# Optimization experiments

Hardware: AMD Instinct MI355X
Metric: run time of the kernel (lower is better)

Reference implementation:

```python
import jax, jax.numpy as jnp
import numpy as np

EMBED_DIM = 1024
HEAD_SIZE = 64
B, T = 4, 4096


def setup_inputs() -> dict:
    key = jax.random.key(0)
    kx, kq, kk, kv = jax.random.split(key, 4)
    x = jax.random.normal(kx, (B, T, EMBED_DIM), dtype=jnp.float32)
    sw = 1.0 / np.sqrt(EMBED_DIM)  # kaiming-ish init scale for linear weights
    Wq = jax.random.normal(kq, (EMBED_DIM, HEAD_SIZE), dtype=jnp.float32) * sw
    Wk = jax.random.normal(kk, (EMBED_DIM, HEAD_SIZE), dtype=jnp.float32) * sw
    Wv = jax.random.normal(kv, (EMBED_DIM, HEAD_SIZE), dtype=jnp.float32) * sw
    return {"x": x, "Wq": Wq, "Wk": Wk, "Wv": Wv}


def reference(x, Wq, Wk, Wv):
    Bn, Tn, C = x.shape
    q = jnp.einsum('btc,ch->bth', x, Wq)
    k = jnp.einsum('btc,ch->bth', x, Wk)
    v = jnp.einsum('btc,ch->bth', x, Wv)
    # NOTE: original scales by sqrt(C) = sqrt(embed_dim), not sqrt(head_size)
    scale = 1.0 / jnp.sqrt(jnp.asarray(C, dtype=x.dtype))
    wei = jnp.einsum('bth,bsh->bts', q, k) * scale  # [B, T, T]
    causal = jnp.tril(jnp.ones((Tn, Tn), dtype=bool))
    wei = jnp.where(causal, wei, -jnp.inf)
    wei = jax.nn.softmax(wei, axis=-1)
    # dropout p=0.0 (eval mode): identity
    return jnp.einsum('bts,bsh->bth', wei, v)
```

## Files before the change

kernel.cpp:

```cpp
#include <hip/hip_runtime.h>
#include <cstdint>


typedef __bf16 bf16;
typedef __bf16 bf16x4 __attribute__((ext_vector_type(4)));
typedef __bf16 bf16x8 __attribute__((ext_vector_type(8)));
typedef float  f32x4  __attribute__((ext_vector_type(4)));

#define MFMA16(a, b, c) __builtin_amdgcn_mfma_f32_16x16x32_bf16((a), (b), (c), 0, 0, 0)

#if __has_builtin(__builtin_amdgcn_exp2f)
#define EXP2(x) __builtin_amdgcn_exp2f(x)
#else
#define EXP2(x) exp2f(x)
#endif

#define B_SZ 4
#define T_SZ 4096
#define C_SZ 1024
#define H_SZ 64
#define M_SZ (B_SZ * T_SZ)
#define QSCALE (1.4426950408889634f / 32.0f)
#define P_O 8192
#define P_L 128

__device__ __forceinline__ void dma16(const void* g, void* l) {
    __builtin_amdgcn_global_load_lds(
        (const __attribute__((address_space(1))) uint32_t*)(uintptr_t)g,
        (__attribute__((address_space(3))) uint32_t*)(uint32_t)(uintptr_t)l,
        16, 0, 0);
}

#define WAIT_BARRIER(N) do {                                       \
    asm volatile("s_waitcnt vmcnt(" #N ")" ::: "memory");          \
    __builtin_amdgcn_s_barrier();                                  \
    __builtin_amdgcn_sched_barrier(0);                             \
} while (0)

#define BOT_BARRIER() do {                                         \
    __builtin_amdgcn_sched_barrier(0);                             \
    __builtin_amdgcn_s_barrier();                                  \
    __builtin_amdgcn_sched_barrier(0);                             \
} while (0)

__global__ __launch_bounds__(256) void wt_prep(
    const float* __restrict__ Wq, const float* __restrict__ Wk,
    const float* __restrict__ Wv, bf16* __restrict__ wt2)
{
    const int n4 = blockIdx.x, t = threadIdx.x;
    const int nbase = n4 * 4;
    const float* W = (nbase < 64) ? Wq : (nbase < 128 ? Wk : Wv);
    const float sc = (nbase < 64) ? QSCALE : 1.0f;
    const int ncol = nbase & 63;
    #pragma unroll
    for (int i = 0; i < 4; ++i) {
        const int k = i * 256 + t;
        const float4 v = *(const float4*)(W + (size_t)k * H_SZ + ncol);
        const float vals[4] = {v.x, v.y, v.z, v.w};
        const size_t base = (size_t)(k >> 6) * 12288 + (size_t)((k >> 5) & 1) * 6144
                          + (size_t)((k >> 3) & 3) * 1536 + (k & 7);
        #pragma unroll
        for (int m = 0; m < 4; ++m)
            wt2[base + (size_t)(nbase + m) * 8] = (bf16)(vals[m] * sc);
    }
}

__global__ __launch_bounds__(512) void qkv_proj(
    const float* __restrict__ x, const bf16* __restrict__ wt2,
    bf16* __restrict__ qw, bf16* __restrict__ kw2, bf16* __restrict__ vtw2)
{
    const int m0 = blockIdx.x * 64;
    const int tid = threadIdx.x;
    const int wave = tid >> 6, lane = tid & 63;
    const int quad = lane >> 4, l15 = lane & 15;
    const int rh = wave >> 2;
    const int cg = wave & 3;
    const int phase = blockIdx.x & 15;

    __shared__ __align__(16) float xs[2][64 * 64];
    __shared__ __align__(16) bf16  ws[2][2 * 4 * 192 * 8];

    f32x4 acc[2][3] = {};

    const int r0 = tid >> 4;
    const int csrc = (tid & 15) ^ (r0 & 7);
    const char* xg0 = (const char*)x + (size_t)(m0 + r0) * 4096 + (size_t)csrc * 16;
    const char* xg1 = xg0 + (size_t)32 * 4096;
    const char* wg = (const char*)wt2 + (size_t)tid * 16;

    auto stage = [&](int s, int buf) {
        const size_t se = (size_t)((s + phase) & 15);
        char* xl = (char*)(&xs[buf][0]) + (size_t)tid * 16;
        char* wl = (char*)(&ws[buf][0]) + (size_t)tid * 16;
        dma16(xg0 + se * 256, xl);
        dma16(xg1 + se * 256, xl + 8192);
        #pragma unroll
        for (int i = 0; i < 3; ++i)
            dma16(wg + se * 24576 + (size_t)i * 8192, wl + (size_t)i * 8192);
    };

    stage(0, 0);

    for (int s = 0; s < 16; ++s) {
        if (s < 15) {
            stage(s + 1, (s + 1) & 1);
            WAIT_BARRIER(5);
        } else {
            WAIT_BARRIER(0);
        }
        const float* xb = &xs[s & 1][0];
        const bf16*  wb = &ws[s & 1][0];

        #pragma unroll
        for (int ss = 0; ss < 2; ++ss) {
            bf16x8 a[2];
            const int cbase = ss * 8 + quad * 2;
            #pragma unroll
            for (int mg = 0; mg < 2; ++mg) {
                const int row = rh * 32 + mg * 16 + l15;
                const int rx = row & 7;
                const float* xrow = xb + row * 64;
                const f32x4 lo = *(const f32x4*)(xrow + ((cbase ^ rx) << 2));
                const f32x4 hi = *(const f32x4*)(xrow + (((cbase + 1) ^ rx) << 2));
                a[mg][0] = (bf16)lo[0]; a[mg][1] = (bf16)lo[1];
                a[mg][2] = (bf16)lo[2]; a[mg][3] = (bf16)lo[3];
                a[mg][4] = (bf16)hi[0]; a[mg][5] = (bf16)hi[1];
                a[mg][6] = (bf16)hi[2]; a[mg][7] = (bf16)hi[3];
            }
            #pragma unroll
            for (int i = 0; i < 3; ++i) {
                const int nt = cg * 3 + i;
                const bf16x8 wf = *(const bf16x8*)(wb + ss * 6144 + quad * 1536
                                                   + (nt * 16 + l15) * 8);
                #pragma unroll
                for (int mg = 0; mg < 2; ++mg)
                    acc[mg][i] = MFMA16(a[mg], wf, acc[mg][i]);
            }
        }

        BOT_BARRIER();
    }

    #pragma unroll
    for (int mg = 0; mg < 2; ++mg)
        #pragma unroll
        for (int i = 0; i < 3; ++i) {
            const int n = (cg * 3 + i) * 16 + l15;
            const int which = n >> 6, col = n & 63;
            #pragma unroll
            for (int r = 0; r < 4; ++r) {
                const int t = m0 + rh * 32 + mg * 16 + quad * 4 + r;
                const bf16 v = (bf16)acc[mg][i][r];
                if (which == 0) {
                    qw[(size_t)t * H_SZ + col] = v;
                } else if (which == 1) {
                    kw2[(size_t)(t >> 6) * 4096
                        + (size_t)(((col >> 5) << 2) + ((col >> 3) & 3)) * 512
                        + (size_t)(t & 63) * 8 + (col & 7)] = v;
                } else {
                    const int t6 = t & 63;
                    const int p = ((t6 >> 2) & 3) * 8 + (t6 & 3) * 2
                                + ((t6 >> 4) & 1) + (t6 >> 5) * 32;
                    vtw2[(size_t)(t >> 6) * 4096
                         + (size_t)(p >> 3) * 512 + (size_t)col * 8 + (p & 7)] = v;
                }
            }
        }
}

__global__ __launch_bounds__(256) void flash_attn(
    const bf16* __restrict__ qw, const bf16* __restrict__ kw2,
    const bf16* __restrict__ vtw2, bf16* __restrict__ pbuf_o,
    float* __restrict__ pbuf_l)
{
    const int bx = blockIdx.x;
    const int item = (bx & 1) ? (511 - (bx >> 1)) : (bx >> 1);
    const int qt2 = 31 - (item >> 4);
    const int b   = (item >> 2) & 3;
    const int h   = item & 3;
    const int i0  = qt2 * 128;
    const int nkv = qt2 * 2 + 2;
    const int n   = (nkv > h) ? ((nkv - 1 - h) >> 2) + 1 : 0;

    const int tid = threadIdx.x;
    const int wave = tid >> 6, lane = tid & 63;
    const int quad = lane >> 4, l15 = lane & 15;

    __shared__ __align__(16) bf16 kvs[2][2][8192];

    bf16x8 aq[2][2];
    #pragma unroll
    for (int mg2 = 0; mg2 < 2; ++mg2) {
        const bf16* qp = qw + ((size_t)b * T_SZ + i0 + wave * 32 + mg2 * 16 + l15) * H_SZ
                       + quad * 8;
        aq[mg2][0] = *(const bf16x8*)qp;
        aq[mg2][1] = *(const bf16x8*)(qp + 32);
    }
    const bf16 onev = (bf16)1.0f;
    const bf16x8 vone = {onev, onev, onev, onev, onev, onev, onev, onev};

    const char* kgb = (const char*)kw2 + (size_t)b * 524288;
    const char* vgb = (const char*)vtw2 + (size_t)b * 524288;

    f32x4 o[2][4] = {};
    f32x4 osum[2] = {};

    auto stage = [&](int k, int buf, int sub) {
        const int jt = h + 4 * k;
        const char* ks = kgb + (size_t)jt * 8192;
        const char* vs = vgb + (size_t)jt * 8192;
        char* dst = (char*)(&kvs[buf][sub][0]) + (size_t)tid * 16;
        dma16(ks + (size_t)tid * 16, dst);
        dma16(ks + 4096 + (size_t)tid * 16, dst + 4096);
        dma16(vs + (size_t)tid * 16, dst + 8192);
        dma16(vs + 4096 + (size_t)tid * 16, dst + 12288);
    };

    auto compute = [&](int k, int buf, int sub) {
        const int jt = h + 4 * k;
        const bf16* kb = &kvs[buf][sub][0];
        const bf16* vb = kb + 4096;

        f32x4 s4t[4][2] = {};
        __builtin_amdgcn_s_setprio(1);
        #pragma unroll
        for (int ct = 0; ct < 4; ++ct) {
            const bf16x8 k0 = *(const bf16x8*)(kb + (0 * 4 + quad) * 512 + (ct * 16 + l15) * 8);
            const bf16x8 k1 = *(const bf16x8*)(kb + (1 * 4 + quad) * 512 + (ct * 16 + l15) * 8);
            #pragma unroll
            for (int mg2 = 0; mg2 < 2; ++mg2) {
                s4t[ct][mg2] = MFMA16(k0, aq[mg2][0], s4t[ct][mg2]);
                s4t[ct][mg2] = MFMA16(k1, aq[mg2][1], s4t[ct][mg2]);
            }
        }
        __builtin_amdgcn_s_setprio(0);

        if (jt >= 2 * qt2) {
            #pragma unroll
            for (int mg2 = 0; mg2 < 2; ++mg2) {
                const int gq = i0 + wave * 32 + mg2 * 16 + l15;
                #pragma unroll
                for (int ct = 0; ct < 4; ++ct) {
                    const int gkv0 = jt * 64 + ct * 16 + quad * 4;
                    #pragma unroll
                    for (int rr = 0; rr < 4; ++rr)
                        if (gkv0 + rr > gq) s4t[ct][mg2][rr] = -3.0e38f;
                }
            }
        }

        bf16x8 pa[2][2];
        #pragma unroll
        for (int mg2 = 0; mg2 < 2; ++mg2)
            #pragma unroll
            for (int j = 0; j < 8; ++j) {
                pa[mg2][0][j] = (bf16)EXP2(s4t[j & 1][mg2][j >> 1]);
                pa[mg2][1][j] = (bf16)EXP2(s4t[2 + (j & 1)][mg2][j >> 1]);
            }

        __builtin_amdgcn_s_setprio(1);
        #pragma unroll
        for (int ht = 0; ht < 4; ++ht) {
            const bf16x8 v0 = *(const bf16x8*)(vb + (0 * 4 + quad) * 512 + (ht * 16 + l15) * 8);
            const bf16x8 v1 = *(const bf16x8*)(vb + (1 * 4 + quad) * 512 + (ht * 16 + l15) * 8);
            #pragma unroll
            for (int mg2 = 0; mg2 < 2; ++mg2) {
                o[mg2][ht] = MFMA16(pa[mg2][0], v0, o[mg2][ht]);
                o[mg2][ht] = MFMA16(pa[mg2][1], v1, o[mg2][ht]);
            }
        }
        #pragma unroll
        for (int mg2 = 0; mg2 < 2; ++mg2) {
            osum[mg2] = MFMA16(pa[mg2][0], vone, osum[mg2]);
            osum[mg2] = MFMA16(pa[mg2][1], vone, osum[mg2]);
        }
        __builtin_amdgcn_s_setprio(0);
    };

    if (n > 0) stage(0, 0, 0);
    if (n > 1) stage(1, 0, 1);

    int c = 0;
    for (int i = 0; i < n; i += 2, c ^= 1) {
        if (i + 3 < n) {
            stage(i + 2, c ^ 1, 0); stage(i + 3, c ^ 1, 1);
            WAIT_BARRIER(8);
        } else if (i + 2 < n) {
            stage(i + 2, c ^ 1, 0);
            WAIT_BARRIER(4);
        } else {
            WAIT_BARRIER(0);
        }
        compute(i, c, 0);
        if (i + 1 < n) compute(i + 1, c, 1);
        BOT_BARRIER();
    }

    bf16* pb_o = pbuf_o + (size_t)(((b * 32 + qt2) * 4) + h) * P_O;
    float* pb_l = pbuf_l + (size_t)(((b * 32 + qt2) * 4) + h) * P_L;
    #pragma unroll
    for (int mg2 = 0; mg2 < 2; ++mg2) {
        const int L0 = wave * 32 + mg2 * 16 + quad * 4;
        #pragma unroll
        for (int ht = 0; ht < 4; ++ht)
            #pragma unroll
            for (int rr = 0; rr < 4; ++rr)
                pb_o[(L0 + rr) * 64 + ht * 16 + l15] = (bf16)o[mg2][ht][rr];
        if (l15 == 0) {
            #pragma unroll
            for (int rr = 0; rr < 4; ++rr)
                pb_l[L0 + rr] = osum[mg2][rr];
        }
    }
}

__global__ __launch_bounds__(256) void combine(
    const bf16* __restrict__ pbuf_o, const float* __restrict__ pbuf_l,
    float* __restrict__ out)
{
    const int bq2 = blockIdx.x >> 1, tid = threadIdx.x;
    const int row = ((blockIdx.x & 1) << 6) + (tid >> 2);
    const int c0 = (tid & 3) * 16;

    float a[16] = {};
    float l = 0.f;
    #pragma unroll
    for (int h = 0; h < 4; ++h) {
        const bf16* ph = pbuf_o + (size_t)(bq2 * 4 + h) * P_O + row * 64 + c0;
        const bf16x8 v0 = *(const bf16x8*)ph;
        const bf16x8 v1 = *(const bf16x8*)(ph + 8);
        #pragma unroll
        for (int j = 0; j < 8; ++j) {
            a[j]     += (float)v0[j];
            a[8 + j] += (float)v1[j];
        }
        l += pbuf_l[(size_t)(bq2 * 4 + h) * P_L + row];
    }
    const float inv = 1.0f / l;
    float* op = out + ((size_t)bq2 * 128 + row) * 64 + c0;
    #pragma unroll
    for (int g = 0; g < 4; ++g) {
        f32x4 v = {a[g * 4], a[g * 4 + 1], a[g * 4 + 2], a[g * 4 + 3]};
        *(f32x4*)(op + g * 4) = v * inv;
    }
}

extern "C" void kernel_launch(void* const* d_in, const int* in_sizes, int n_in,
                              void* d_out, int out_size, void* d_ws, size_t ws_size,
                              hipStream_t stream) {
    const float* x  = (const float*)d_in[0];
    const float* Wq = (const float*)d_in[1];
    const float* Wk = (const float*)d_in[2];
    const float* Wv = (const float*)d_in[3];

    bf16* qw   = (bf16*)d_ws;
    bf16* kw2  = qw + (size_t)M_SZ * H_SZ;
    bf16* vtw2 = kw2 + (size_t)M_SZ * H_SZ;
    bf16* wt2  = vtw2 + (size_t)M_SZ * H_SZ;
    bf16* pbuf_o = wt2 + 3 * 64 * 1024;
    float* pbuf_l = (float*)(pbuf_o + (size_t)512 * P_O);
    float* out = (float*)d_out;

    wt_prep<<<48, 256, 0, stream>>>(Wq, Wk, Wv, wt2);
    qkv_proj<<<M_SZ / 64, 512, 0, stream>>>(x, wt2, qw, kw2, vtw2);
    flash_attn<<<512, 256, 0, stream>>>(qw, kw2, vtw2, pbuf_o, pbuf_l);
    combine<<<256, 256, 0, stream>>>(pbuf_o, pbuf_l, out);
}
```

Baseline: 132.7 us.

## Convert x tiles to bf16 in registers before LDS store in QKV projection

The QKV projection now loads fp32 x tiles into registers two stages ahead, converts them to bf16 and writes them to LDS with a swizzle, instead of DMA-ing fp32 into LDS and converting on every fragment read. This halves the LDS footprint and read bandwidth for x and removes repeated conversions inside the MFMA loop. In exchange it uses a register-staged pipeline with manual waitcnt and barrier placement, which adds register pressure and relies on the hand-counted vmcnt values being correct.

```diff
diff --git a/kernel.cpp b/kernel.cpp
--- a/kernel.cpp
+++ b/kernel.cpp
@@ -77,68 +77,87 @@
     const int cg = wave & 3;
     const int phase = blockIdx.x & 15;
 
-    __shared__ __align__(16) float xs[2][64 * 64];
-    __shared__ __align__(16) bf16  ws[2][2 * 4 * 192 * 8];
+    __shared__ __align__(16) bf16 xs[2][64 * 64];
+    __shared__ __align__(16) bf16 ws[2][2 * 4 * 192 * 8];
 
     f32x4 acc[2][3] = {};
 
     const int r0 = tid >> 4;
-    const int csrc = (tid & 15) ^ (r0 & 7);
-    const char* xg0 = (const char*)x + (size_t)(m0 + r0) * 4096 + (size_t)csrc * 16;
+    const int hh = tid & 15;
+    const char* xg0 = (const char*)x + (size_t)(m0 + r0) * 4096 + (size_t)hh * 16;
     const char* xg1 = xg0 + (size_t)32 * 4096;
     const char* wg = (const char*)wt2 + (size_t)tid * 16;
-
-    auto stage = [&](int s, int buf) {
+    const int xo0 = r0 * 128 + (((hh >> 1) ^ (r0 & 7)) << 4) + ((hh & 1) << 3);
+    const int xo1 = xo0 + 32 * 128;
+
+    auto stage_w = [&](int s, int buf) {
         const size_t se = (size_t)((s + phase) & 15);
-        char* xl = (char*)(&xs[buf][0]) + (size_t)tid * 16;
         char* wl = (char*)(&ws[buf][0]) + (size_t)tid * 16;
-        dma16(xg0 + se * 256, xl);
-        dma16(xg1 + se * 256, xl + 8192);
         #pragma unroll
         for (int i = 0; i < 3; ++i)
             dma16(wg + se * 24576 + (size_t)i * 8192, wl + (size_t)i * 8192);
     };
-
-    stage(0, 0);
+    auto load_x = [&](int s, float4& A, float4& B) {
+        const size_t se = (size_t)((s + phase) & 15);
+        A = *(const float4*)(xg0 + se * 256);
+        B = *(const float4*)(xg1 + se * 256);
+    };
+    auto write_x = [&](const float4& A, const float4& B, int buf) {
+        bf16x4 c0, c1;
+        c0[0] = (bf16)A.x; c0[1] = (bf16)A.y; c0[2] = (bf16)A.z; c0[3] = (bf16)A.w;
+        c1[0] = (bf16)B.x; c1[1] = (bf16)B.y; c1[2] = (bf16)B.z; c1[3] = (bf16)B.w;
+        *(bf16x4*)((char*)(&xs[buf][0]) + xo0) = c0;
+        *(bf16x4*)((char*)(&xs[buf][0]) + xo1) = c1;
+    };
+
+    float4 xb0, xb1;
+    {
+        float4 p0, p1;
+        load_x(0, p0, p1);
+        write_x(p0, p1, 0);
+        stage_w(0, 0);
+        load_x(1, xb0, xb1);
+    }
 
     for (int s = 0; s < 16; ++s) {
-        if (s < 15) {
-            stage(s + 1, (s + 1) & 1);
-            WAIT_BARRIER(5);
+        if (s == 15) {
+            asm volatile("s_waitcnt vmcnt(0) lgkmcnt(0)" ::: "memory");
         } else {
-            WAIT_BARRIER(0);
-        }
-        const float* xb = &xs[s & 1][0];
-        const bf16*  wb = &ws[s & 1][0];
+            asm volatile("s_waitcnt vmcnt(2) lgkmcnt(0)" ::: "memory");
+        }
+        __builtin_amdgcn_s_barrier();
+        __builtin_amdgcn_sched_barrier(0);
+
+        if (s < 15) stage_w(s + 1, (s + 1) & 1);
+        float4 nx0, nx1;
+        if (s < 14) load_x(s + 2, nx0, nx1);
+
+        const bf16* xb = &xs[s & 1][0];
+        const bf16* wb = &ws[s & 1][0];
 
         #pragma unroll
         for (int ss = 0; ss < 2; ++ss) {
             bf16x8 a[2];
-            const int cbase = ss * 8 + quad * 2;
             #pragma unroll
             for (int mg = 0; mg < 2; ++mg) {
                 const int row = rh * 32 + mg * 16 + l15;
-                const int rx = row & 7;
-                const float* xrow = xb + row * 64;
-                const f32x4 lo = *(const f32x4*)(xrow + ((cbase ^ rx) << 2));
-                const f32x4 hi = *(const f32x4*)(xrow + (((cbase + 1) ^ rx) << 2));
-                a[mg][0] = (bf16)lo[0]; a[mg][1] = (bf16)lo[1];
-                a[mg][2] = (bf16)lo[2]; a[mg][3] = (bf16)lo[3];
-                a[mg][4] = (bf16)hi[0]; a[mg][5] = (bf16)hi[1];
-                a[mg][6] = (bf16)hi[2]; a[mg][7] = (bf16)hi[3];
+                a[mg] = *(const bf16x8*)((const char*)xb + row * 128
+                          + (((ss * 4 + quad) ^ (row & 7)) << 4));
             }
             #pragma unroll
             for (int i = 0; i < 3; ++i) {
-                const int nt = cg * 3 + i;
                 const bf16x8 wf = *(const bf16x8*)(wb + ss * 6144 + quad * 1536
-                                                   + (nt * 16 + l15) * 8);
+                                                   + ((cg * 3 + i) * 16 + l15) * 8);
                 #pragma unroll
                 for (int mg = 0; mg < 2; ++mg)
                     acc[mg][i] = MFMA16(a[mg], wf, acc[mg][i]);
             }
         }
 
-        BOT_BARRIER();
+        __builtin_amdgcn_sched_barrier(0);
+        if (s < 15) write_x(xb0, xb1, (s + 1) & 1);
+        if (s < 14) { xb0 = nx0; xb1 = nx1; }
+        __builtin_amdgcn_sched_barrier(0);
     }
 
     #pragma unroll
```

After: 135.3 us. About the same (+1.9%).
